# Kernel optimization log

Measured on AMD Instinct MI355X. Metric: run time of the kernel, lower is better.

## Reference

```python
import jax, jax.numpy as jnp
import numpy as np

E = 1024
M = 6
GH = 256
FR = 16  # FiLM bottleneck r = max(16, E//64)


def setup_inputs() -> dict:
    key = jax.random.key(0)
    ks = jax.random.split(key, 32)
    n = lambda k, shape, std=0.02: jax.random.normal(k, shape, dtype=jnp.float32) * std
    inp = {
        "x": jax.random.normal(ks[0], (4, 2048, E), dtype=jnp.float32),
        # gate MLP E->GH->M
        "gw1": n(ks[1], (E, GH)), "gb1": jnp.zeros((GH,), jnp.float32),
        "gw2": n(ks[2], (GH, M)), "gb2": jnp.zeros((M,), jnp.float32),
        "ebias": jnp.zeros((M,), jnp.float32),
        "pm_alpha": jnp.float32(0.5),
        # expert 0: DoubleMLP E->2E->E
        "dfc_w": n(ks[3], (E, 2 * E)), "dfc_b": jnp.zeros((2 * E,), jnp.float32),
        "dproj_w": n(ks[4], (2 * E, E)), "dproj_b": jnp.zeros((E,), jnp.float32),
        # expert 1: SingleMLP E->E->E
        "sfc_w": n(ks[5], (E, E)), "sfc_b": jnp.zeros((E,), jnp.float32),
        "sproj_w": n(ks[6], (E, E)), "sproj_b": jnp.zeros((E,), jnp.float32),
        # expert 2: rank-2 perceptron
        "p2_w": n(ks[7], (2, E)), "p2_v": n(ks[8], (2, E)),
        "p2_alpha": jnp.ones((2,), jnp.float32), "p2_b": jnp.zeros((2,), jnp.float32),
        "p2_bias": jnp.zeros((E,), jnp.float32),
        # expert 3: rank-4 perceptron
        "p4_w": n(ks[9], (4, E)), "p4_v": n(ks[10], (4, E)),
        "p4_alpha": jnp.ones((4,), jnp.float32), "p4_b": jnp.zeros((4,), jnp.float32),
        "p4_bias": jnp.zeros((E,), jnp.float32),
        # expert 4: ReGLU1D
        "rg_u": n(ks[11], (E,)), "rg_a": jnp.ones((E,), jnp.float32),
        "rg_b": jnp.zeros((1,), jnp.float32), "rg_bias": jnp.zeros((E,), jnp.float32),
        # expert 5: FiLM E->FR->2E
        "fl_dw": n(ks[12], (E, FR)), "fl_db": jnp.zeros((FR,), jnp.float32),
        "fl_uw": n(ks[13], (FR, 2 * E)), "fl_ub": jnp.zeros((2 * E,), jnp.float32),
    }
    return inp


def _gelu(x):
    return jax.nn.gelu(x, approximate=False)  # torch nn.GELU default (erf)


def _rank_n(x, w, v, alpha, b, biasvec):
    # y = biasvec + sum_i alpha_i * gelu(<w_i,x> + b_i) * v_i
    s = jnp.einsum("bse,ne->bsn", x, w) + b
    g = _gelu(s)
    return jnp.einsum("bsn,ne->bse", alpha * g, v) + biasvec


def reference(x, gw1, gb1, gw2, gb2, ebias, pm_alpha,
              dfc_w, dfc_b, dproj_w, dproj_b,
              sfc_w, sfc_b, sproj_w, sproj_b,
              p2_w, p2_v, p2_alpha, p2_b, p2_bias,
              p4_w, p4_v, p4_alpha, p4_b, p4_bias,
              rg_u, rg_a, rg_b, rg_bias,
              fl_dw, fl_db, fl_uw, fl_ub):
    # gate logits [B,S,M]; tau=1.0
    gl = _gelu(x @ gw1 + gb1) @ gw2 + gb2 + ebias
    pi = jax.nn.softmax(gl, axis=-1)
    # top_k=1 sparse weights: mask to top-1 then renormalize
    _, topi = jax.lax.top_k(pi, 1)
    mask = jax.nn.one_hot(topi[..., 0], M, dtype=pi.dtype)
    w = pi * mask
    w = w / (jnp.sum(w, axis=-1, keepdims=True) + 1e-9)

    # experts (dropout = identity in eval)
    o0 = _gelu(x @ dfc_w + dfc_b) @ dproj_w + dproj_b            # DoubleMLP
    o1 = _gelu(x @ sfc_w + sfc_b) @ sproj_w + sproj_b            # SingleMLP
    o2 = _rank_n(x, p2_w, p2_v, p2_alpha, p2_b, p2_bias)          # perc2
    o3 = _rank_n(x, p4_w, p4_v, p4_alpha, p4_b, p4_bias)          # perc4
    s = x @ rg_u + rg_b[0]                                        # ReGLU1D
    o4 = jax.nn.sigmoid(s)[..., None] * (x * rg_a) + rg_bias
    t = _gelu(x @ fl_dw + fl_db)                                  # FiLM
    gb = t @ fl_uw + fl_ub
    gamma, beta = jnp.split(gb, 2, axis=-1)
    o5 = gamma * x + beta

    all_out = jnp.stack([o0, o1, o2, o3, o4, o5], axis=-1)        # [B,S,E,M]
    mixed = jnp.sum(all_out * w[..., None, :], axis=-1)
    return pm_alpha * mixed
```

## Files before the change

kernel.cpp:

```cpp
#include <hip/hip_runtime.h>
#include <math.h>


#define E 1024
#define GH 256
#define NEXP 6
#define NTOK 8192

typedef __attribute__((ext_vector_type(8))) short bf16x8;
typedef __attribute__((ext_vector_type(4))) float f32x4;

__device__ __forceinline__ float gelu_erf(float v) {
    return 0.5f * v * (1.0f + erff(v * 0.70710678118654752440f));
}

__device__ __forceinline__ unsigned short f2bf(float f) {
    union { float f; unsigned u; } c; c.f = f;
    unsigned u = c.u;
    u += 0x7fffu + ((u >> 16) & 1u);
    return (unsigned short)(u >> 16);
}

__device__ __forceinline__ float bf2f(unsigned short h) {
    union { unsigned u; float f; } c; c.u = ((unsigned)h) << 16;
    return c.f;
}

__device__ __forceinline__ int ldso(int row, int q) {
    return row * 32 + ((q ^ ((row >> 1) & 3)) << 3);
}

__global__ __launch_bounds__(256)
void prep_kernel(const float* __restrict__ x, unsigned short* __restrict__ xh,
                 unsigned short* __restrict__ xl,
                 const float* __restrict__ gw1, unsigned short* __restrict__ w1cat,
                 const float* __restrict__ fl_dw, float* __restrict__ fl_dwT,
                 const float* __restrict__ dfc_w, unsigned short* __restrict__ dfc_wt,
                 const float* __restrict__ dproj_w, unsigned short* __restrict__ dpj_wt,
                 const float* __restrict__ sfc_w, unsigned short* __restrict__ sfc_wt,
                 const float* __restrict__ sproj_w, unsigned short* __restrict__ spj_wt) {
    __shared__ float tile[32][33];
    const int tid = threadIdx.x;
    const int tx = tid & 31, ty = tid >> 5;
    int b = blockIdx.x;
    if (b < 2048) {
        const int n4 = NTOK * E / 4;
        for (int i = b * 256 + tid; i < n4; i += 2048 * 256) {
            float4 v = reinterpret_cast<const float4*>(x)[i];
            ushort4 h, l;
            h.x = f2bf(v.x); l.x = f2bf(v.x - bf2f(h.x));
            h.y = f2bf(v.y); l.y = f2bf(v.y - bf2f(h.y));
            h.z = f2bf(v.z); l.z = f2bf(v.z - bf2f(h.z));
            h.w = f2bf(v.w); l.w = f2bf(v.w - bf2f(h.w));
            reinterpret_cast<ushort4*>(xh)[i] = h;
            reinterpret_cast<ushort4*>(xl)[i] = l;
        }
        return;
    }
    b -= 2048;
    if (b < 256) {
        const int c0 = (b & 7) * 32, r0 = (b >> 3) * 32;
#pragma unroll
        for (int i = 0; i < 4; ++i)
            tile[ty + i * 8][tx] = gw1[(size_t)(r0 + ty + i * 8) * GH + c0 + tx];
        __syncthreads();
#pragma unroll
        for (int i = 0; i < 4; ++i) {
            float v = tile[tx][ty + i * 8];
            unsigned short h = f2bf(v);
            size_t row = (size_t)(c0 + ty + i * 8) * 2048;
            w1cat[row + r0 + tx] = h;
            w1cat[row + 1024 + r0 + tx] = f2bf(v - bf2f(h));
        }
        return;
    }
    b -= 256;
    if (b < 64) {
        int idx = b * 256 + tid;
        int j = idx >> 10, k = idx & (E - 1);
        fl_dwT[idx] = fl_dw[k * 16 + j];
        return;
    }
    b -= 64;
    const float* src; unsigned short* dst; int R, C, nbx;
    if (b < 2048)      { src = dfc_w;   dst = dfc_wt; R = 1024; C = 2048; nbx = 64; }
    else if (b < 4096) { src = dproj_w; dst = dpj_wt; R = 2048; C = 1024; nbx = 32; b -= 2048; }
    else if (b < 5120) { src = sfc_w;   dst = sfc_wt; R = 1024; C = 1024; nbx = 32; b -= 4096; }
    else               { src = sproj_w; dst = spj_wt; R = 1024; C = 1024; nbx = 32; b -= 5120; }
    const int c0 = (b % nbx) * 32, r0 = (b / nbx) * 32;
#pragma unroll
    for (int i = 0; i < 4; ++i)
        tile[ty + i * 8][tx] = src[(size_t)(r0 + ty + i * 8) * C + c0 + tx];
    __syncthreads();
#pragma unroll
    for (int i = 0; i < 4; ++i)
        dst[(size_t)(c0 + ty + i * 8) * R + r0 + tx] = f2bf(tile[tx][ty + i * 8]);
}

__global__ __launch_bounds__(256)
void gate_partial_kernel(const unsigned short* __restrict__ xh,
                         const unsigned short* __restrict__ xl,
                         const unsigned short* __restrict__ w1cat,
                         float* __restrict__ hp0, float* __restrict__ hp1) {
    __shared__ __align__(16) unsigned short As[128 * 32];
    __shared__ __align__(16) unsigned short Bs[64 * 32];
    const int tid = threadIdx.x;
    const int t0 = blockIdx.y * 128, n0 = blockIdx.x * 64, z = blockIdx.z;
    const unsigned short* A = z ? xl : xh;
    float* hp = z ? hp1 : hp0;

    const int lane = tid & 63, wv = tid >> 6;
    const int wm = (wv & 1) * 64, wn = (wv >> 1) * 32;
    const int lm = lane & 15, q = lane >> 4;
    const int r0 = tid >> 2, gsl = tid & 3;
    const int g = gsl ^ ((r0 >> 1) & 3);

    const unsigned short* pa0 = A + (size_t)(t0 + r0) * E + g * 8;
    const unsigned short* pa1 = A + (size_t)(t0 + r0 + 64) * E + g * 8;
    const unsigned short* pb0 = w1cat + (size_t)(n0 + r0) * 2048 + g * 8;

    f32x4 acc[4][2];
#pragma unroll
    for (int s = 0; s < 4; ++s)
#pragma unroll
        for (int t = 0; t < 2; ++t) acc[s][t] = (f32x4){0.f, 0.f, 0.f, 0.f};

    bf16x8 ra0 = *(const bf16x8*)(pa0);
    bf16x8 ra1 = *(const bf16x8*)(pa1);
    bf16x8 rb0 = *(const bf16x8*)(pb0);
    *(bf16x8*)&As[r0 * 32 + gsl * 8] = ra0;
    *(bf16x8*)&As[(r0 + 64) * 32 + gsl * 8] = ra1;
    *(bf16x8*)&Bs[r0 * 32 + gsl * 8] = rb0;

    int k0 = 0;
    while (true) {
        __syncthreads();
        const int kn = k0 + 32;
        if (kn < 2048) {
            ra0 = *(const bf16x8*)(pa0 + (kn & 1023));
            ra1 = *(const bf16x8*)(pa1 + (kn & 1023));
            rb0 = *(const bf16x8*)(pb0 + kn);
        }
        bf16x8 af[4], bf[2];
#pragma unroll
        for (int s = 0; s < 4; ++s) af[s] = *(const bf16x8*)&As[ldso(wm + s * 16 + lm, q)];
#pragma unroll
        for (int t = 0; t < 2; ++t) bf[t] = *(const bf16x8*)&Bs[ldso(wn + t * 16 + lm, q)];
#pragma unroll
        for (int s = 0; s < 4; ++s)
#pragma unroll
            for (int t = 0; t < 2; ++t)
                acc[s][t] = __builtin_amdgcn_mfma_f32_16x16x32_bf16(af[s], bf[t], acc[s][t], 0, 0, 0);
        if (kn >= 2048) break;
        __syncthreads();
        *(bf16x8*)&As[r0 * 32 + gsl * 8] = ra0;
        *(bf16x8*)&As[(r0 + 64) * 32 + gsl * 8] = ra1;
        *(bf16x8*)&Bs[r0 * 32 + gsl * 8] = rb0;
        k0 = kn;
    }
#pragma unroll
    for (int s = 0; s < 4; ++s)
#pragma unroll
        for (int t = 0; t < 2; ++t)
#pragma unroll
            for (int rg = 0; rg < 4; ++rg) {
                int rl = wm + s * 16 + q * 4 + rg;
                int c  = wn + t * 16 + lm;
                hp[(size_t)(t0 + rl) * GH + n0 + c] = acc[s][t][rg];
            }
}

__global__ __launch_bounds__(256)
void gate_finalize_kernel(const float* __restrict__ hp0, const float* __restrict__ hp1,
                          const float* __restrict__ gb1, const float* __restrict__ gw2,
                          const float* __restrict__ gb2, const float* __restrict__ ebias,
                          const float* __restrict__ pm_alpha,
                          float* __restrict__ scale, int* __restrict__ counts,
                          int* __restrict__ tlist, int* __restrict__ eid) {
    __shared__ float hs[32][264];
    __shared__ float g2s[GH * NEXP];
    __shared__ int tokexp[32];
    const int tid = threadIdx.x;
    const int t0 = blockIdx.x * 32;
    for (int i = tid; i < GH * NEXP; i += 256) g2s[i] = gw2[i];
#pragma unroll
    for (int i = 0; i < 8; ++i) {
        int f4 = i * 256 + tid;
        int row = f4 >> 6, c4 = (f4 & 63) * 4;
        size_t base = (size_t)(t0 + row) * GH + c4;
        float4 a = *reinterpret_cast<const float4*>(&hp0[base]);
        float4 b = *reinterpret_cast<const float4*>(&hp1[base]);
        float4 o;
        o.x = gelu_erf(a.x + b.x + gb1[c4 + 0]);
        o.y = gelu_erf(a.y + b.y + gb1[c4 + 1]);
        o.z = gelu_erf(a.z + b.z + gb1[c4 + 2]);
        o.w = gelu_erf(a.w + b.w + gb1[c4 + 3]);
        *reinterpret_cast<float4*>(&hs[row][c4]) = o;
    }
    __syncthreads();
    const int t = tid >> 3, j = tid & 7;
    float p[NEXP] = {0.f, 0.f, 0.f, 0.f, 0.f, 0.f};
#pragma unroll 8
    for (int kk = 0; kk < 32; ++kk) {
        int k = j + kk * 8;
        float hv = hs[t][k];
        const float* gr = &g2s[k * NEXP];
#pragma unroll
        for (int m = 0; m < NEXP; ++m) p[m] += hv * gr[m];
    }
#pragma unroll
    for (int m = 0; m < NEXP; ++m) {
        p[m] += __shfl_xor(p[m], 4, 64);
        p[m] += __shfl_xor(p[m], 2, 64);
        p[m] += __shfl_xor(p[m], 1, 64);
    }
    if (j == 0) {
        float L[NEXP];
#pragma unroll
        for (int m = 0; m < NEXP; ++m) L[m] = p[m] + gb2[m] + ebias[m];
        float mx = L[0]; int am = 0;
#pragma unroll
        for (int m = 1; m < NEXP; ++m) { if (L[m] > mx) { mx = L[m]; am = m; } }
        float S = 0.f;
#pragma unroll
        for (int m = 0; m < NEXP; ++m) S += expf(L[m] - mx);
        float pt = 1.f / S;
        scale[t0 + t] = pm_alpha[0] * (pt / (pt + 1e-9f));
        eid[t0 + t] = am;
        tokexp[t] = am;
    }
    __syncthreads();
    if (tid < NEXP) {
        const int e = tid;
        int cnt = 0;
#pragma unroll
        for (int i = 0; i < 32; ++i) cnt += (tokexp[i] == e);
        if (cnt) {
            int base = atomicAdd(&counts[e], cnt);
            int pos = 0;
#pragma unroll
            for (int i = 0; i < 32; ++i)
                if (tokexp[i] == e) tlist[e * NTOK + base + (pos++)] = t0 + i;
        }
    }
}

__global__ __launch_bounds__(256)
void moe_gemm1_kernel(const unsigned short* __restrict__ xh,
                      const unsigned short* __restrict__ B0, const unsigned short* __restrict__ B1,
                      const float* __restrict__ bias0, const float* __restrict__ bias1,
                      const int* __restrict__ counts, const int* __restrict__ tlist,
                      unsigned short* __restrict__ H0, unsigned short* __restrict__ H1) {
    const int z = blockIdx.z;
    const int N = z ? 1024 : 2048;
    const int K = E;
    const int cnt = counts[z];
    const int i0 = blockIdx.y * 64;
    const int n0 = blockIdx.x * 128;
    if (i0 >= cnt || n0 >= N) return;
    const unsigned short* Bz = z ? B1 : B0;
    const float* bias = z ? bias1 : bias0;

    __shared__ __align__(16) unsigned short As[64 * 32];
    __shared__ __align__(16) unsigned short Bs[128 * 32];
    __shared__ int toks[64];
    const int tid = threadIdx.x;
    if (tid < 64) toks[tid] = tlist[z * NTOK + min(i0 + tid, cnt - 1)];
    __syncthreads();

    const int lane = tid & 63, wv = tid >> 6;
    const int wm = (wv & 1) * 32, wn = (wv >> 1) * 64;
    const int lm = lane & 15, q = lane >> 4;
    const int r0 = tid >> 2, gsl = tid & 3;
    const int g = gsl ^ ((r0 >> 1) & 3);

    const unsigned short* pa = xh + (size_t)toks[r0] * K + g * 8;
    const unsigned short* pb0 = Bz + (size_t)(n0 + r0) * K + g * 8;
    const unsigned short* pb1 = Bz + (size_t)(n0 + r0 + 64) * K + g * 8;

    f32x4 acc[2][4];
#pragma unroll
    for (int s = 0; s < 2; ++s)
#pragma unroll
        for (int t = 0; t < 4; ++t) acc[s][t] = (f32x4){0.f, 0.f, 0.f, 0.f};

    bf16x8 ra  = *(const bf16x8*)(pa);
    bf16x8 rb0 = *(const bf16x8*)(pb0);
    bf16x8 rb1 = *(const bf16x8*)(pb1);
    *(bf16x8*)&As[r0 * 32 + gsl * 8] = ra;
    *(bf16x8*)&Bs[r0 * 32 + gsl * 8] = rb0;
    *(bf16x8*)&Bs[(r0 + 64) * 32 + gsl * 8] = rb1;

    int k0 = 0;
    while (true) {
        __syncthreads();
        const int kn = k0 + 32;
        if (kn < K) {
            ra  = *(const bf16x8*)(pa + kn);
            rb0 = *(const bf16x8*)(pb0 + kn);
            rb1 = *(const bf16x8*)(pb1 + kn);
        }
        bf16x8 af[2], bf[4];
#pragma unroll
        for (int s = 0; s < 2; ++s) af[s] = *(const bf16x8*)&As[ldso(wm + s * 16 + lm, q)];
#pragma unroll
        for (int t = 0; t < 4; ++t) bf[t] = *(const bf16x8*)&Bs[ldso(wn + t * 16 + lm, q)];
#pragma unroll
        for (int s = 0; s < 2; ++s)
#pragma unroll
            for (int t = 0; t < 4; ++t)
                acc[s][t] = __builtin_amdgcn_mfma_f32_16x16x32_bf16(af[s], bf[t], acc[s][t], 0, 0, 0);
        if (kn >= K) break;
        __syncthreads();
        *(bf16x8*)&As[r0 * 32 + gsl * 8] = ra;
        *(bf16x8*)&Bs[r0 * 32 + gsl * 8] = rb0;
        *(bf16x8*)&Bs[(r0 + 64) * 32 + gsl * 8] = rb1;
        k0 = kn;
    }
    unsigned short* Hz = z ? H1 : H0;
#pragma unroll
    for (int s = 0; s < 2; ++s)
#pragma unroll
        for (int t = 0; t < 4; ++t)
#pragma unroll
            for (int rg = 0; rg < 4; ++rg) {
                int rl = wm + s * 16 + q * 4 + rg;
                int gc = n0 + wn + t * 16 + lm;
                float v = acc[s][t][rg] + bias[gc];
                Hz[(size_t)(i0 + rl) * N + gc] = f2bf(gelu_erf(v));
            }
}

__global__ __launch_bounds__(256)
void gemm2_cheap_kernel(const unsigned short* __restrict__ h1, const unsigned short* __restrict__ h2,
                        const unsigned short* __restrict__ dpj, const unsigned short* __restrict__ spj,
                        const float* __restrict__ dproj_b, const float* __restrict__ sproj_b,
                        const int* __restrict__ counts, const int* __restrict__ tlist,
                        const float* __restrict__ scale,
                        const float* __restrict__ x, const int* __restrict__ eid,
                        const float* __restrict__ p2_w, const float* __restrict__ p2_v,
                        const float* __restrict__ p2_alpha, const float* __restrict__ p2_b,
                        const float* __restrict__ p2_bias,
                        const float* __restrict__ p4_w, const float* __restrict__ p4_v,
                        const float* __restrict__ p4_alpha, const float* __restrict__ p4_b,
                        const float* __restrict__ p4_bias,
                        const float* __restrict__ rg_u, const float* __restrict__ rg_a,
                        const float* __restrict__ rg_b, const float* __restrict__ rg_bias,
                        const float* __restrict__ fl_dwT, const float* __restrict__ fl_db,
                        const float* __restrict__ fl_uw, const float* __restrict__ fl_ub,
                        float* __restrict__ out) {
    __shared__ __align__(16) char smem[64 * 32 * 2 + 128 * 32 * 2 + 64 * 4];
    const int tid = threadIdx.x;
    const int bb = blockIdx.x;

    if (bb < 512) {
        const int z = bb >> 8;
        const int r = bb & 255;
        const int n0 = (r & 7) * 128;
        const int i0 = (r >> 3) * 64;
        const int K = z ? 1024 : 2048;
        const int cnt = counts[z];
        if (i0 >= cnt) return;
        const int rows = min(64, cnt - i0);
        const unsigned short* Az = z ? h2 : h1;
        const unsigned short* Bz = z ? spj : dpj;
        const float* bias = z ? sproj_b : dproj_b;

        unsigned short* As = (unsigned short*)smem;
        unsigned short* Bs = As + 64 * 32;
        int* toks = (int*)(Bs + 128 * 32);
        if (tid < 64) toks[tid] = tlist[z * NTOK + min(i0 + tid, cnt - 1)];
        __syncthreads();

        const int lane = tid & 63, wv = tid >> 6;
        const int wm = (wv & 1) * 32, wn = (wv >> 1) * 64;
        const int lm = lane & 15, q = lane >> 4;
        const int r0 = tid >> 2, gsl = tid & 3;
        const int g = gsl ^ ((r0 >> 1) & 3);

        const unsigned short* pa = Az + (size_t)(i0 + r0) * K + g * 8;
        const unsigned short* pb0 = Bz + (size_t)(n0 + r0) * K + g * 8;
        const unsigned short* pb1 = Bz + (size_t)(n0 + r0 + 64) * K + g * 8;

        f32x4 acc[2][4];
#pragma unroll
        for (int s = 0; s < 2; ++s)
#pragma unroll
            for (int t = 0; t < 4; ++t) acc[s][t] = (f32x4){0.f, 0.f, 0.f, 0.f};

        bf16x8 ra  = *(const bf16x8*)(pa);
        bf16x8 rb0 = *(const bf16x8*)(pb0);
        bf16x8 rb1 = *(const bf16x8*)(pb1);
        *(bf16x8*)&As[r0 * 32 + gsl * 8] = ra;
        *(bf16x8*)&Bs[r0 * 32 + gsl * 8] = rb0;
        *(bf16x8*)&Bs[(r0 + 64) * 32 + gsl * 8] = rb1;

        int k0 = 0;
        while (true) {
            __syncthreads();
            const int kn = k0 + 32;
            if (kn < K) {
                ra  = *(const bf16x8*)(pa + kn);
                rb0 = *(const bf16x8*)(pb0 + kn);
                rb1 = *(const bf16x8*)(pb1 + kn);
            }
            bf16x8 af[2], bf[4];
#pragma unroll
            for (int s = 0; s < 2; ++s) af[s] = *(const bf16x8*)&As[ldso(wm + s * 16 + lm, q)];
#pragma unroll
            for (int t = 0; t < 4; ++t) bf[t] = *(const bf16x8*)&Bs[ldso(wn + t * 16 + lm, q)];
#pragma unroll
            for (int s = 0; s < 2; ++s)
#pragma unroll
                for (int t = 0; t < 4; ++t)
                    acc[s][t] = __builtin_amdgcn_mfma_f32_16x16x32_bf16(af[s], bf[t], acc[s][t], 0, 0, 0);
            if (kn >= K) break;
            __syncthreads();
            *(bf16x8*)&As[r0 * 32 + gsl * 8] = ra;
            *(bf16x8*)&Bs[r0 * 32 + gsl * 8] = rb0;
            *(bf16x8*)&Bs[(r0 + 64) * 32 + gsl * 8] = rb1;
            k0 = kn;
        }
#pragma unroll
        for (int s = 0; s < 2; ++s)
#pragma unroll
            for (int t = 0; t < 4; ++t)
#pragma unroll
                for (int rg = 0; rg < 4; ++rg) {
                    int rl = wm + s * 16 + q * 4 + rg;
                    if (rl < rows) {
                        int gc = n0 + wn + t * 16 + lm;
                        int tok = toks[rl];
                        out[(size_t)tok * E + gc] = scale[tok] * (acc[s][t][rg] + bias[gc]);
                    }
                }
        return;
    }

    const int tok = bb - 512;
    const int e = eid[tok];
    if (e < 2) return;
    float* xs  = (float*)smem;
    float* red = xs + E;
    float* gs  = red + 64;
    *reinterpret_cast<float4*>(&xs[tid * 4]) =
        *reinterpret_cast<const float4*>(&x[(size_t)tok * E + tid * 4]);
    __syncthreads();
    const float sc = scale[tok];
    const int lane = tid & 63, wid = tid >> 6;

    if (e == 2 || e == 3) {
        const int n = (e == 2) ? 2 : 4;
        const float* w    = (e == 2) ? p2_w : p4_w;
        const float* v    = (e == 2) ? p2_v : p4_v;
        const float* al   = (e == 2) ? p2_alpha : p4_alpha;
        const float* b    = (e == 2) ? p2_b : p4_b;
        const float* bias = (e == 2) ? p2_bias : p4_bias;
        float p[4] = {0.f, 0.f, 0.f, 0.f};
        for (int k = tid; k < E; k += 256) {
            float xv = xs[k];
            for (int j = 0; j < n; ++j) p[j] += xv * w[j * E + k];
        }
        for (int j = 0; j < n; ++j) {
            float val = p[j];
            for (int off = 32; off > 0; off >>= 1) val += __shfl_down(val, off, 64);
            if (lane == 0) red[j * 4 + wid] = val;
        }
        __syncthreads();
        if (tid < n) {
            float s = red[tid * 4] + red[tid * 4 + 1] + red[tid * 4 + 2] + red[tid * 4 + 3] + b[tid];
            gs[tid] = al[tid] * gelu_erf(s);
        }
        __syncthreads();
        for (int cx = tid; cx < E; cx += 256) {
            float o = bias[cx];
            for (int j = 0; j < n; ++j) o += gs[j] * v[j * E + cx];
            out[(size_t)tok * E + cx] = sc * o;
        }
    } else if (e == 4) {
        float pv = 0.f;
        for (int k = tid; k < E; k += 256) pv += xs[k] * rg_u[k];
        for (int off = 32; off > 0; off >>= 1) pv += __shfl_down(pv, off, 64);
        if (lane == 0) red[wid] = pv;
        __syncthreads();
        float s = red[0] + red[1] + red[2] + red[3] + rg_b[0];
        float sg = 1.f / (1.f + expf(-s));
        for (int cx = tid; cx < E; cx += 256)
            out[(size_t)tok * E + cx] = sc * (sg * xs[cx] * rg_a[cx] + rg_bias[cx]);
    } else {
        float p[16];
#pragma unroll
        for (int j = 0; j < 16; ++j) p[j] = 0.f;
        for (int k = tid; k < E; k += 256) {
            float xv = xs[k];
#pragma unroll
            for (int j = 0; j < 16; ++j) p[j] += xv * fl_dwT[j * E + k];
        }
#pragma unroll
        for (int j = 0; j < 16; ++j) {
            float val = p[j];
            for (int off = 32; off > 0; off >>= 1) val += __shfl_down(val, off, 64);
            if (lane == 0) red[j * 4 + wid] = val;
        }
        __syncthreads();
        if (tid < 16)
            gs[tid] = gelu_erf(red[tid * 4] + red[tid * 4 + 1] + red[tid * 4 + 2] + red[tid * 4 + 3] + fl_db[tid]);
        __syncthreads();
        for (int cx = tid; cx < E; cx += 256) {
            float ga = fl_ub[cx], be = fl_ub[E + cx];
#pragma unroll
            for (int j = 0; j < 16; ++j) {
                float tj = gs[j];
                ga += tj * fl_uw[j * 2 * E + cx];
                be += tj * fl_uw[j * 2 * E + E + cx];
            }
            out[(size_t)tok * E + cx] = sc * (ga * xs[cx] + be);
        }
    }
}

extern "C" void kernel_launch(void* const* d_in, const int* in_sizes, int n_in,
                              void* d_out, int out_size, void* d_ws, size_t ws_size,
                              hipStream_t stream) {
    const float* x        = (const float*)d_in[0];
    const float* gw1      = (const float*)d_in[1];
    const float* gb1      = (const float*)d_in[2];
    const float* gw2      = (const float*)d_in[3];
    const float* gb2      = (const float*)d_in[4];
    const float* ebias    = (const float*)d_in[5];
    const float* pm_alpha = (const float*)d_in[6];
    const float* dfc_w    = (const float*)d_in[7];
    const float* dfc_b    = (const float*)d_in[8];
    const float* dproj_w  = (const float*)d_in[9];
    const float* dproj_b  = (const float*)d_in[10];
    const float* sfc_w    = (const float*)d_in[11];
    const float* sfc_b    = (const float*)d_in[12];
    const float* sproj_w  = (const float*)d_in[13];
    const float* sproj_b  = (const float*)d_in[14];
    const float* p2_w     = (const float*)d_in[15];
    const float* p2_v     = (const float*)d_in[16];
    const float* p2_alpha = (const float*)d_in[17];
    const float* p2_b     = (const float*)d_in[18];
    const float* p2_bias  = (const float*)d_in[19];
    const float* p4_w     = (const float*)d_in[20];
    const float* p4_v     = (const float*)d_in[21];
    const float* p4_alpha = (const float*)d_in[22];
    const float* p4_b     = (const float*)d_in[23];
    const float* p4_bias  = (const float*)d_in[24];
    const float* rg_u     = (const float*)d_in[25];
    const float* rg_a     = (const float*)d_in[26];
    const float* rg_b     = (const float*)d_in[27];
    const float* rg_bias  = (const float*)d_in[28];
    const float* fl_dw    = (const float*)d_in[29];
    const float* fl_db    = (const float*)d_in[30];
    const float* fl_uw    = (const float*)d_in[31];
    const float* fl_ub    = (const float*)d_in[32];
    float* out = (float*)d_out;

    char* ws = (char*)d_ws;
    size_t off = 0;
    int*            counts = (int*)(ws + off);            off += 256;
    float*          scale  = (float*)(ws + off);          off += (size_t)NTOK * 4;
    int*            tlist  = (int*)(ws + off);            off += (size_t)NEXP * NTOK * 4;
    int*            eid    = (int*)(ws + off);            off += (size_t)NTOK * 4;
    float*          fl_dwT = (float*)(ws + off);          off += (size_t)16 * E * 4;
    unsigned short* w1cat  = (unsigned short*)(ws + off); off += (size_t)GH * 2048 * 2;
    unsigned short* dfc_wt = (unsigned short*)(ws + off); off += (size_t)2048 * 1024 * 2;
    unsigned short* dpj_wt = (unsigned short*)(ws + off); off += (size_t)1024 * 2048 * 2;
    unsigned short* sfc_wt = (unsigned short*)(ws + off); off += (size_t)1024 * 1024 * 2;
    unsigned short* spj_wt = (unsigned short*)(ws + off); off += (size_t)1024 * 1024 * 2;
    unsigned short* x_hi   = (unsigned short*)(ws + off); off += (size_t)NTOK * E * 2;
    char* U = ws + off;
    unsigned short* x_lo = (unsigned short*)U;
    float*          hp0  = (float*)(U + (size_t)16 * 1024 * 1024);
    float*          hp1  = (float*)(U + (size_t)24 * 1024 * 1024);
    unsigned short* h1   = (unsigned short*)U;
    unsigned short* h2   = (unsigned short*)(U + (size_t)16 * 1024 * 1024);

    hipMemsetAsync(counts, 0, 256, stream);
    prep_kernel<<<8512, 256, 0, stream>>>(x, x_hi, x_lo, gw1, w1cat, fl_dw, fl_dwT,
                                          dfc_w, dfc_wt, dproj_w, dpj_wt,
                                          sfc_w, sfc_wt, sproj_w, spj_wt);
    gate_partial_kernel<<<dim3(GH / 64, NTOK / 128, 2), 256, 0, stream>>>(x_hi, x_lo, w1cat, hp0, hp1);
    gate_finalize_kernel<<<NTOK / 32, 256, 0, stream>>>(hp0, hp1, gb1, gw2, gb2, ebias,
                                                        pm_alpha, scale, counts, tlist, eid);
    moe_gemm1_kernel<<<dim3(16, 32, 2), 256, 0, stream>>>(
        x_hi, dfc_wt, sfc_wt, dfc_b, sfc_b, counts, tlist, h1, h2);
    gemm2_cheap_kernel<<<512 + NTOK, 256, 0, stream>>>(
        h1, h2, dpj_wt, spj_wt, dproj_b, sproj_b, counts, tlist, scale,
        x, eid,
        p2_w, p2_v, p2_alpha, p2_b, p2_bias,
        p4_w, p4_v, p4_alpha, p4_b, p4_bias,
        rg_u, rg_a, rg_b, rg_bias,
        fl_dwT, fl_db, fl_uw, fl_ub, out);
    (void)in_sizes; (void)n_in; (void)out_size; (void)ws_size;
}
```

Before: 299.8 us.

## Shrink MoE GEMM tiles to 64x64 and vectorize cheap-expert per-token path

Both expert GEMM kernels move from 64x128 to 64x64 output tiles, doubling the grid so that more blocks are in flight when only a few tokens route to the MLP experts. In exchange, each block reuses the A tile across fewer columns and issues fewer MFMAs per sync. The cheap-expert path now has each thread load one float4 of x directly into registers, dropping the shared-memory staging and its barrier, and writes one float4 of output per thread with vectorized weight loads.

Measured after the change: 297.9 us. No clear change (-0.6%).

```diff
diff --git a/kernel.cpp b/kernel.cpp
--- a/kernel.cpp
+++ b/kernel.cpp
@@ -24,6 +24,10 @@
 __device__ __forceinline__ float bf2f(unsigned short h) {
     union { unsigned u; float f; } c; c.u = ((unsigned)h) << 16;
     return c.f;
+}
+
+__device__ __forceinline__ float dot4(float4 a, float4 b) {
+    return a.x * b.x + a.y * b.y + a.z * b.z + a.w * b.w;
 }
 
 __device__ __forceinline__ int ldso(int row, int q) {
@@ -256,72 +260,67 @@
     const int K = E;
     const int cnt = counts[z];
     const int i0 = blockIdx.y * 64;
-    const int n0 = blockIdx.x * 128;
+    const int n0 = blockIdx.x * 64;
     if (i0 >= cnt || n0 >= N) return;
     const unsigned short* Bz = z ? B1 : B0;
     const float* bias = z ? bias1 : bias0;
 
     __shared__ __align__(16) unsigned short As[64 * 32];
-    __shared__ __align__(16) unsigned short Bs[128 * 32];
+    __shared__ __align__(16) unsigned short Bs[64 * 32];
     __shared__ int toks[64];
     const int tid = threadIdx.x;
     if (tid < 64) toks[tid] = tlist[z * NTOK + min(i0 + tid, cnt - 1)];
     __syncthreads();
 
     const int lane = tid & 63, wv = tid >> 6;
-    const int wm = (wv & 1) * 32, wn = (wv >> 1) * 64;
+    const int wm = (wv & 1) * 32, wn = (wv >> 1) * 32;
     const int lm = lane & 15, q = lane >> 4;
     const int r0 = tid >> 2, gsl = tid & 3;
     const int g = gsl ^ ((r0 >> 1) & 3);
 
     const unsigned short* pa = xh + (size_t)toks[r0] * K + g * 8;
-    const unsigned short* pb0 = Bz + (size_t)(n0 + r0) * K + g * 8;
-    const unsigned short* pb1 = Bz + (size_t)(n0 + r0 + 64) * K + g * 8;
-
-    f32x4 acc[2][4];
+    const unsigned short* pb = Bz + (size_t)(n0 + r0) * K + g * 8;
+
+    f32x4 acc[2][2];
 #pragma unroll
     for (int s = 0; s < 2; ++s)
 #pragma unroll
-        for (int t = 0; t < 4; ++t) acc[s][t] = (f32x4){0.f, 0.f, 0.f, 0.f};
-
-    bf16x8 ra  = *(const bf16x8*)(pa);
-    bf16x8 rb0 = *(const bf16x8*)(pb0);
-    bf16x8 rb1 = *(const bf16x8*)(pb1);
+        for (int t = 0; t < 2; ++t) acc[s][t] = (f32x4){0.f, 0.f, 0.f, 0.f};
+
+    bf16x8 ra = *(const bf16x8*)(pa);
+    bf16x8 rb = *(const bf16x8*)(pb);
     *(bf16x8*)&As[r0 * 32 + gsl * 8] = ra;
-    *(bf16x8*)&Bs[r0 * 32 + gsl * 8] = rb0;
-    *(bf16x8*)&Bs[(r0 + 64) * 32 + gsl * 8] = rb1;
+    *(bf16x8*)&Bs[r0 * 32 + gsl * 8] = rb;
 
     int k0 = 0;
     while (true) {
         __syncthreads();
         const int kn = k0 + 32;
         if (kn < K) {
-            ra  = *(const bf16x8*)(pa + kn);
-            rb0 = *(const bf16x8*)(pb0 + kn);
-            rb1 = *(const bf16x8*)(pb1 + kn);
-        }
-        bf16x8 af[2], bf[4];
+            ra = *(const bf16x8*)(pa + kn);
+            rb = *(const bf16x8*)(pb + kn);
+        }
+        bf16x8 af[2], bf[2];
 #pragma unroll
         for (int s = 0; s < 2; ++s) af[s] = *(const bf16x8*)&As[ldso(wm + s * 16 + lm, q)];
 #pragma unroll
-        for (int t = 0; t < 4; ++t) bf[t] = *(const bf16x8*)&Bs[ldso(wn + t * 16 + lm, q)];
+        for (int t = 0; t < 2; ++t) bf[t] = *(const bf16x8*)&Bs[ldso(wn + t * 16 + lm, q)];
 #pragma unroll
         for (int s = 0; s < 2; ++s)
 #pragma unroll
-            for (int t = 0; t < 4; ++t)
+            for (int t = 0; t < 2; ++t)
                 acc[s][t] = __builtin_amdgcn_mfma_f32_16x16x32_bf16(af[s], bf[t], acc[s][t], 0, 0, 0);
         if (kn >= K) break;
         __syncthreads();
         *(bf16x8*)&As[r0 * 32 + gsl * 8] = ra;
-        *(bf16x8*)&Bs[r0 * 32 + gsl * 8] = rb0;
-        *(bf16x8*)&Bs[(r0 + 64) * 32 + gsl * 8] = rb1;
+        *(bf16x8*)&Bs[r0 * 32 + gsl * 8] = rb;
         k0 = kn;
     }
     unsigned short* Hz = z ? H1 : H0;
 #pragma unroll
     for (int s = 0; s < 2; ++s)
 #pragma unroll
-        for (int t = 0; t < 4; ++t)
+        for (int t = 0; t < 2; ++t)
 #pragma unroll
             for (int rg = 0; rg < 4; ++rg) {
                 int rl = wm + s * 16 + q * 4 + rg;
@@ -349,15 +348,15 @@
                         const float* __restrict__ fl_dwT, const float* __restrict__ fl_db,
                         const float* __restrict__ fl_uw, const float* __restrict__ fl_ub,
                         float* __restrict__ out) {
-    __shared__ __align__(16) char smem[64 * 32 * 2 + 128 * 32 * 2 + 64 * 4];
+    __shared__ __align__(16) char smem[64 * 32 * 2 * 2 + 64 * 4];
     const int tid = threadIdx.x;
     const int bb = blockIdx.x;
 
-    if (bb < 512) {
-        const int z = bb >> 8;
-        const int r = bb & 255;
-        const int n0 = (r & 7) * 128;
-        const int i0 = (r >> 3) * 64;
+    if (bb < 1024) {
+        const int z = bb >> 9;
+        const int r = bb & 511;
+        const int n0 = (r & 15) * 64;
+        const int i0 = (r >> 4) * 64;
         const int K = z ? 1024 : 2048;
         const int cnt = counts[z];
         if (i0 >= cnt) return;
@@ -368,63 +367,58 @@
 
         unsigned short* As = (unsigned short*)smem;
         unsigned short* Bs = As + 64 * 32;
-        int* toks = (int*)(Bs + 128 * 32);
+        int* toks = (int*)(Bs + 64 * 32);
         if (tid < 64) toks[tid] = tlist[z * NTOK + min(i0 + tid, cnt - 1)];
         __syncthreads();
 
         const int lane = tid & 63, wv = tid >> 6;
-        const int wm = (wv & 1) * 32, wn = (wv >> 1) * 64;
+        const int wm = (wv & 1) * 32, wn = (wv >> 1) * 32;
         const int lm = lane & 15, q = lane >> 4;
         const int r0 = tid >> 2, gsl = tid & 3;
         const int g = gsl ^ ((r0 >> 1) & 3);
 
         const unsigned short* pa = Az + (size_t)(i0 + r0) * K + g * 8;
-        const unsigned short* pb0 = Bz + (size_t)(n0 + r0) * K + g * 8;
-        const unsigned short* pb1 = Bz + (size_t)(n0 + r0 + 64) * K + g * 8;
-
-        f32x4 acc[2][4];
+        const unsigned short* pb = Bz + (size_t)(n0 + r0) * K + g * 8;
+
+        f32x4 acc[2][2];
 #pragma unroll
         for (int s = 0; s < 2; ++s)
 #pragma unroll
-            for (int t = 0; t < 4; ++t) acc[s][t] = (f32x4){0.f, 0.f, 0.f, 0.f};
-
-        bf16x8 ra  = *(const bf16x8*)(pa);
-        bf16x8 rb0 = *(const bf16x8*)(pb0);
-        bf16x8 rb1 = *(const bf16x8*)(pb1);
+            for (int t = 0; t < 2; ++t) acc[s][t] = (f32x4){0.f, 0.f, 0.f, 0.f};
+
+        bf16x8 ra = *(const bf16x8*)(pa);
+        bf16x8 rb = *(const bf16x8*)(pb);
         *(bf16x8*)&As[r0 * 32 + gsl * 8] = ra;
-        *(bf16x8*)&Bs[r0 * 32 + gsl * 8] = rb0;
-        *(bf16x8*)&Bs[(r0 + 64) * 32 + gsl * 8] = rb1;
+        *(bf16x8*)&Bs[r0 * 32 + gsl * 8] = rb;
 
         int k0 = 0;
         while (true) {
             __syncthreads();
             const int kn = k0 + 32;
             if (kn < K) {
-                ra  = *(const bf16x8*)(pa + kn);
-                rb0 = *(const bf16x8*)(pb0 + kn);
-                rb1 = *(const bf16x8*)(pb1 + kn);
+                ra = *(const bf16x8*)(pa + kn);
+                rb = *(const bf16x8*)(pb + kn);
             }
-            bf16x8 af[2], bf[4];
+            bf16x8 af[2], bf[2];
 #pragma unroll
             for (int s = 0; s < 2; ++s) af[s] = *(const bf16x8*)&As[ldso(wm + s * 16 + lm, q)];
 #pragma unroll
-            for (int t = 0; t < 4; ++t) bf[t] = *(const bf16x8*)&Bs[ldso(wn + t * 16 + lm, q)];
+            for (int t = 0; t < 2; ++t) bf[t] = *(const bf16x8*)&Bs[ldso(wn + t * 16 + lm, q)];
 #pragma unroll
             for (int s = 0; s < 2; ++s)
 #pragma unroll
-                for (int t = 0; t < 4; ++t)
+                for (int t = 0; t < 2; ++t)
                     acc[s][t] = __builtin_amdgcn_mfma_f32_16x16x32_bf16(af[s], bf[t], acc[s][t], 0, 0, 0);
             if (kn >= K) break;
             __syncthreads();
             *(bf16x8*)&As[r0 * 32 + gsl * 8] = ra;
-            *(bf16x8*)&Bs[r0 * 32 + gsl * 8] = rb0;
-            *(bf16x8*)&Bs[(r0 + 64) * 32 + gsl * 8] = rb1;
+            *(bf16x8*)&Bs[r0 * 32 + gsl * 8] = rb;
             k0 = kn;
         }
 #pragma unroll
         for (int s = 0; s < 2; ++s)
 #pragma unroll
-            for (int t = 0; t < 4; ++t)
+            for (int t = 0; t < 2; ++t)
 #pragma unroll
                 for (int rg = 0; rg < 4; ++rg) {
                     int rl = wm + s * 16 + q * 4 + rg;
@@ -437,17 +431,16 @@
         return;
     }
 
-    const int tok = bb - 512;
+    const int tok = bb - 1024;
     const int e = eid[tok];
     if (e < 2) return;
-    float* xs  = (float*)smem;
-    float* red = xs + E;
+    float* red = (float*)smem;
     float* gs  = red + 64;
-    *reinterpret_cast<float4*>(&xs[tid * 4]) =
-        *reinterpret_cast<const float4*>(&x[(size_t)tok * E + tid * 4]);
-    __syncthreads();
+    const int k4 = tid * 4;
+    const float4 xv = *reinterpret_cast<const float4*>(&x[(size_t)tok * E + k4]);
     const float sc = scale[tok];
     const int lane = tid & 63, wid = tid >> 6;
+    float4 o;
 
     if (e == 2 || e == 3) {
         const int n = (e == 2) ? 2 : 4;
@@ -456,13 +449,8 @@
         const float* al   = (e == 2) ? p2_alpha : p4_alpha;
         const float* b    = (e == 2) ? p2_b : p4_b;
         const float* bias = (e == 2) ? p2_bias : p4_bias;
-        float p[4] = {0.f, 0.f, 0.f, 0.f};
-        for (int k = tid; k < E; k += 256) {
-            float xv = xs[k];
-            for (int j = 0; j < n; ++j) p[j] += xv * w[j * E + k];
-        }
         for (int j = 0; j < n; ++j) {
-            float val = p[j];
+            float val = dot4(xv, *reinterpret_cast<const float4*>(&w[j * E + k4]));
             for (int off = 32; off > 0; off >>= 1) val += __shfl_down(val, off, 64);
             if (lane == 0) red[j * 4 + wid] = val;
         }
@@ -472,33 +460,29 @@
             gs[tid] = al[tid] * gelu_erf(s);
         }
         __syncthreads();
-        for (int cx = tid; cx < E; cx += 256) {
-            float o = bias[cx];
-            for (int j = 0; j < n; ++j) o += gs[j] * v[j * E + cx];
-            out[(size_t)tok * E + cx] = sc * o;
+        o = *reinterpret_cast<const float4*>(&bias[k4]);
+        for (int j = 0; j < n; ++j) {
+            float4 vv = *reinterpret_cast<const float4*>(&v[j * E + k4]);
+            float gj = gs[j];
+            o.x += gj * vv.x; o.y += gj * vv.y; o.z += gj * vv.z; o.w += gj * vv.w;
         }
     } else if (e == 4) {
-        float pv = 0.f;
-        for (int k = tid; k < E; k += 256) pv += xs[k] * rg_u[k];
-        for (int off = 32; off > 0; off >>= 1) pv += __shfl_down(pv, off, 64);
-        if (lane == 0) red[wid] = pv;
+        float val = dot4(xv, *reinterpret_cast<const float4*>(&rg_u[k4]));
+        for (int off = 32; off > 0; off >>= 1) val += __shfl_down(val, off, 64);
+        if (lane == 0) red[wid] = val;
         __syncthreads();
         float s = red[0] + red[1] + red[2] + red[3] + rg_b[0];
         float sg = 1.f / (1.f + expf(-s));
-        for (int cx = tid; cx < E; cx += 256)
-            out[(size_t)tok * E + cx] = sc * (sg * xs[cx] * rg_a[cx] + rg_bias[cx]);
+        float4 av = *reinterpret_cast<const float4*>(&rg_a[k4]);
+        float4 bv = *reinterpret_cast<const float4*>(&rg_bias[k4]);
+        o.x = sg * xv.x * av.x + bv.x;
+        o.y = sg * xv.y * av.y + bv.y;
+        o.z = sg * xv.z * av.z + bv.z;
+        o.w = sg * xv.w * av.w + bv.w;
     } else {
-        float p[16];
-#pragma unroll
-        for (int j = 0; j < 16; ++j) p[j] = 0.f;
-        for (int k = tid; k < E; k += 256) {
-            float xv = xs[k];
-#pragma unroll
-            for (int j = 0; j < 16; ++j) p[j] += xv * fl_dwT[j * E + k];
-        }
 #pragma unroll
         for (int j = 0; j < 16; ++j) {
-            float val = p[j];
+            float val = dot4(xv, *reinterpret_cast<const float4*>(&fl_dwT[j * E + k4]));
             for (int off = 32; off > 0; off >>= 1) val += __shfl_down(val, off, 64);
             if (lane == 0) red[j * 4 + wid] = val;
         }
@@ -506,17 +490,23 @@
         if (tid < 16)
             gs[tid] = gelu_erf(red[tid * 4] + red[tid * 4 + 1] + red[tid * 4 + 2] + red[tid * 4 + 3] + fl_db[tid]);
         __syncthreads();
-        for (int cx = tid; cx < E; cx += 256) {
-            float ga = fl_ub[cx], be = fl_ub[E + cx];
-#pragma unroll
-            for (int j = 0; j < 16; ++j) {
-                float tj = gs[j];
-                ga += tj * fl_uw[j * 2 * E + cx];
-                be += tj * fl_uw[j * 2 * E + E + cx];
-            }
-            out[(size_t)tok * E + cx] = sc * (ga * xs[cx] + be);
-        }
-    }
+        float4 ga = *reinterpret_cast<const float4*>(&fl_ub[k4]);
+        float4 be = *reinterpret_cast<const float4*>(&fl_ub[E + k4]);
+#pragma unroll
+        for (int j = 0; j < 16; ++j) {
+            float tj = gs[j];
+            float4 ug = *reinterpret_cast<const float4*>(&fl_uw[(size_t)j * 2 * E + k4]);
+            float4 ub = *reinterpret_cast<const float4*>(&fl_uw[(size_t)j * 2 * E + E + k4]);
+            ga.x += tj * ug.x; ga.y += tj * ug.y; ga.z += tj * ug.z; ga.w += tj * ug.w;
+            be.x += tj * ub.x; be.y += tj * ub.y; be.z += tj * ub.z; be.w += tj * ub.w;
+        }
+        o.x = ga.x * xv.x + be.x;
+        o.y = ga.y * xv.y + be.y;
+        o.z = ga.z * xv.z + be.z;
+        o.w = ga.w * xv.w + be.w;
+    }
+    o.x *= sc; o.y *= sc; o.z *= sc; o.w *= sc;
+    *reinterpret_cast<float4*>(&out[(size_t)tok * E + k4]) = o;
 }
 
 extern "C" void kernel_launch(void* const* d_in, const int* in_sizes, int n_in,
@@ -584,9 +574,9 @@
     gate_partial_kernel<<<dim3(GH / 64, NTOK / 128, 2), 256, 0, stream>>>(x_hi, x_lo, w1cat, hp0, hp1);
     gate_finalize_kernel<<<NTOK / 32, 256, 0, stream>>>(hp0, hp1, gb1, gw2, gb2, ebias,
                                                         pm_alpha, scale, counts, tlist, eid);
-    moe_gemm1_kernel<<<dim3(16, 32, 2), 256, 0, stream>>>(
+    moe_gemm1_kernel<<<dim3(32, 32, 2), 256, 0, stream>>>(
         x_hi, dfc_wt, sfc_wt, dfc_b, sfc_b, counts, tlist, h1, h2);
-    gemm2_cheap_kernel<<<512 + NTOK, 256, 0, stream>>>(
+    gemm2_cheap_kernel<<<1024 + NTOK, 256, 0, stream>>>(
         h1, h2, dpj_wt, spj_wt, dproj_b, sproj_b, counts, tlist, scale,
         x, eid,
         p2_w, p2_v, p2_alpha, p2_b, p2_bias,
```
